# Performance work log

Measured on AMD Instinct MI355X. Metric: run time of the kernel, lower is better.

The kernel has to match this reference:

```python
import jax, jax.numpy as jnp
import numpy as np
from jax import lax

PRE_NMS_TOPN = 6000
POST_NMS_TOPN = 1500
NMS_IOU_THRESHOLD = 0.7
VARIANCES = (0.1, 0.1, 0.2, 0.2)
TOTAL_ANCHORS = 200000
BATCH = 8


def setup_inputs() -> dict:
    key = jax.random.key(0)
    k1, k2, k3, k4 = jax.random.split(key, 4)
    rpn_bbox_deltas = jax.random.normal(k1, (BATCH, TOTAL_ANCHORS, 4), dtype=jnp.float32)
    rpn_probs = jax.random.uniform(k2, (BATCH, TOTAL_ANCHORS), dtype=jnp.float32)
    # anchors: valid normalized [y1, x1, y2, x2] boxes
    ctr = jax.random.uniform(k3, (TOTAL_ANCHORS, 2), dtype=jnp.float32)          # (cy, cx)
    hw = jax.random.uniform(k4, (TOTAL_ANCHORS, 2), dtype=jnp.float32,
                            minval=0.02, maxval=0.3)                              # (h, w)
    anchors = jnp.concatenate([ctr - 0.5 * hw, ctr + 0.5 * hw], axis=-1)
    return {"rpn_bbox_deltas": rpn_bbox_deltas, "rpn_probs": rpn_probs, "anchors": anchors}


def _nms_single(boxes):
    # boxes: [P, 4] sorted by descending score; greedy NMS, return [POST, 4] zero-padded,
    # coordinates clipped to [0, 1] (tf combined_non_max_suppression clip_boxes=True default).
    P = boxes.shape[0]
    y1, x1, y2, x2 = boxes[:, 0], boxes[:, 1], boxes[:, 2], boxes[:, 3]
    area = (y2 - y1) * (x2 - x1)
    iy1 = jnp.maximum(y1[:, None], y1[None, :])
    ix1 = jnp.maximum(x1[:, None], x1[None, :])
    iy2 = jnp.minimum(y2[:, None], y2[None, :])
    ix2 = jnp.minimum(x2[:, None], x2[None, :])
    inter = jnp.maximum(iy2 - iy1, 0.0) * jnp.maximum(ix2 - ix1, 0.0)
    iou = inter / (area[:, None] + area[None, :] - inter)  # [P, P]
    idx = jnp.arange(P)

    def body(i, keep):
        suppressed = keep[i] & (iou[i] > NMS_IOU_THRESHOLD) & (idx > i)
        return keep & ~suppressed

    keep = lax.fori_loop(0, P, body, jnp.ones((P,), dtype=bool))

    rank = jnp.cumsum(keep) - 1                      # position among kept boxes
    valid = keep & (rank < POST_NMS_TOPN)
    tgt = jnp.where(valid, rank, POST_NMS_TOPN)      # overflow slot for dropped boxes
    clipped = jnp.clip(boxes, 0.0, 1.0)
    out = jnp.zeros((POST_NMS_TOPN + 1, 4), dtype=boxes.dtype)
    out = out.at[tgt].set(jnp.where(valid[:, None], clipped, 0.0))
    return out[:POST_NMS_TOPN]


def reference(rpn_bbox_deltas, rpn_probs, anchors):
    variances = jnp.asarray(VARIANCES, dtype=rpn_bbox_deltas.dtype)
    deltas = rpn_bbox_deltas * variances                       # [B, A, 4]

    anc_w = anchors[:, 3] - anchors[:, 1]
    anc_h = anchors[:, 2] - anchors[:, 0]
    anc_cx = anchors[:, 1] + 0.5 * anc_w
    anc_cy = anchors[:, 0] + 0.5 * anc_h

    bw = jnp.exp(deltas[..., 3]) * anc_w
    bh = jnp.exp(deltas[..., 2]) * anc_h
    bcx = deltas[..., 1] * anc_w + anc_cx
    bcy = deltas[..., 0] * anc_h + anc_cy

    y1 = bcy - 0.5 * bh
    x1 = bcx - 0.5 * bw
    y2 = bh + y1
    x2 = bw + x1
    rpn_bboxes = jnp.stack([y1, x1, y2, x2], axis=-1)          # [B, A, 4]

    _, pre_indices = lax.top_k(rpn_probs, PRE_NMS_TOPN)        # [B, P], sorted desc
    pre_boxes = jnp.take_along_axis(rpn_bboxes, pre_indices[..., None], axis=1)  # [B, P, 4]

    roi_bboxes = jax.vmap(_nms_single)(pre_boxes)              # [B, POST, 4]
    return roi_bboxes
```

## Files before the change

### kernel.cpp

```cpp
#include <hip/hip_runtime.h>
#include <hip/hip_bf16.h>


#define TOTAL   200000
#define NBATCH  8
#define PRE     6000
#define POST    1500
#define NW      94
#define CAP     8192
#define NQ      (TOTAL/4)
#define GR      256
#define NG      24
#define NGFAST  13
#define PLANES  960

__device__ __forceinline__ unsigned int prob_key(float p) {
    return __float_as_uint(__fadd_rn(p, 1.0f)) & 0x7FFFFFu;
}

__global__ __launch_bounds__(1024) void k_hist256(const float* __restrict__ probs,
                                                  unsigned int* __restrict__ hist) {
    const int b = blockIdx.y;
    const int tid = threadIdx.x;
    __shared__ unsigned int h[256];
    if (tid < 256) h[tid] = 0u;
    __syncthreads();
    const float4* p4 = (const float4*)(probs + (size_t)b * TOTAL);
    for (int i4 = blockIdx.x * 1024 + tid; i4 < NQ; i4 += 8 * 1024) {
        float4 v = p4[i4];
        atomicAdd(&h[prob_key(v.x) >> 15], 1u);
        atomicAdd(&h[prob_key(v.y) >> 15], 1u);
        atomicAdd(&h[prob_key(v.z) >> 15], 1u);
        atomicAdd(&h[prob_key(v.w) >> 15], 1u);
    }
    __syncthreads();
    if (tid < 256 && h[tid] > 0u) atomicAdd(&hist[b * 256 + tid], h[tid]);
}

__global__ __launch_bounds__(1024) void k_collect(const float* __restrict__ probs,
                                                  const unsigned int* __restrict__ hist,
                                                  unsigned long long* __restrict__ keys,
                                                  unsigned int* __restrict__ gcount) {
    const int b = blockIdx.y;
    const int tid = threadIdx.x;
    __shared__ unsigned int S[257];
    __shared__ unsigned int lcnt[256];
    __shared__ unsigned int gbase[256];
    __shared__ unsigned int s_B;
    if (tid == 0) { s_B = 0u; S[256] = 0u; }
    if (tid < 256) { S[tid] = hist[b * 256 + tid]; lcnt[tid] = 0u; }
    __syncthreads();
    for (int off = 1; off < 256; off <<= 1) {
        unsigned int v = 0u;
        if (tid < 256 && tid + off < 256) v = S[tid + off];
        __syncthreads();
        if (tid < 256) S[tid] += v;
        __syncthreads();
    }
    if (tid < 256 && S[tid] >= PRE) atomicMax(&s_B, (unsigned int)tid);
    __syncthreads();
    const unsigned int B = s_B;
    unsigned int kk[4], ii[4], tt[4], lp[4]; int n = 0;
    const int i4 = blockIdx.x * 1024 + tid;
    if (i4 < NQ) {
        float4 v = ((const float4*)(probs + (size_t)b * TOTAL))[i4];
        float pv[4] = {v.x, v.y, v.z, v.w};
#pragma unroll
        for (int j = 0; j < 4; ++j) {
            unsigned int key = prob_key(pv[j]);
            unsigned int t = key >> 15;
            if (t >= B) {
                kk[n] = key; ii[n] = (unsigned int)(i4 * 4 + j); tt[n] = t;
                lp[n] = atomicAdd(&lcnt[t], 1u);
                ++n;
            }
        }
    }
    __syncthreads();
    if (tid < 256 && lcnt[tid] > 0u)
        gbase[tid] = atomicAdd(&gcount[b * 256 + tid], lcnt[tid]);
    __syncthreads();
    for (int j = 0; j < n; ++j) {
        unsigned int t = tt[j];
        unsigned int pos = S[t + 1] + gbase[t] + lp[j];
        if (pos < CAP)
            keys[(size_t)b * CAP + pos] =
                ((unsigned long long)kk[j] << 32) | (unsigned long long)(~ii[j]);
    }
}

__global__ __launch_bounds__(256) void k_rank(const unsigned long long* __restrict__ keys,
                                              const unsigned int* __restrict__ hist,
                                              const float* __restrict__ deltas,
                                              const float* __restrict__ anchors,
                                              float4* __restrict__ boxes) {
    const int b   = blockIdx.y;
    const int rel = blockIdx.x;
    const int tid = threadIdx.x;
    __shared__ unsigned int S[257];
    __shared__ unsigned int s_B;
    __shared__ unsigned long long K2[CAP];
    __shared__ unsigned int CNT[512];
    __shared__ unsigned int W[512];
    __shared__ unsigned int P[256];
    if (tid == 0) { s_B = 0u; S[256] = 0u; }
    S[tid] = hist[b * 256 + tid];
    __syncthreads();
    for (int off = 1; off < 256; off <<= 1) {
        unsigned int v = (tid + off < 256) ? S[tid + off] : 0u;
        __syncthreads();
        S[tid] += v;
        __syncthreads();
    }
    if (S[tid] >= PRE) atomicMax(&s_B, (unsigned int)tid);
    __syncthreads();
    const int B = (int)s_B;
    const int t = B + rel;
    if (t > 255) return;
    const unsigned int lo = (rel == 15) ? 0u : S[t + 1];
    unsigned int hi = S[t]; if (hi > CAP) hi = CAP;
    if (hi <= lo) return;
    const unsigned int n = hi - lo;
    CNT[tid] = 0u; CNT[tid + 256] = 0u;
    __syncthreads();
    const unsigned long long* kb = keys + (size_t)b * CAP + lo;
    for (unsigned int i = tid; i < n; i += 256u) {
        const unsigned int key23 = (unsigned int)(kb[i] >> 32);
        const unsigned int bin = (rel == 15) ? (key23 >> 14) : ((key23 >> 6) & 511u);
        atomicAdd(&CNT[bin], 1u);
    }
    __syncthreads();
    {
        const unsigned int c0 = CNT[2 * tid], c1 = CNT[2 * tid + 1];
        P[tid] = c0 + c1;
        __syncthreads();
        for (int off = 1; off < 256; off <<= 1) {
            unsigned int v = (tid + off < 256) ? P[tid + off] : 0u;
            __syncthreads();
            P[tid] += v;
            __syncthreads();
        }
        const unsigned int above = P[tid] - (c0 + c1);
        W[2 * tid + 1] = above;
        W[2 * tid]     = above + c1;
    }
    __syncthreads();
    for (unsigned int i = tid; i < n; i += 256u) {
        const unsigned long long k = kb[i];
        const unsigned int key23 = (unsigned int)(k >> 32);
        const unsigned int bin = (rel == 15) ? (key23 >> 14) : ((key23 >> 6) & 511u);
        const unsigned int slot = atomicAdd(&W[bin], 1u);
        K2[slot] = k;
    }
    __syncthreads();
    for (int s = tid; s < 512; s += 256) {
        const unsigned int st = (s < 511) ? W[s + 1] : 0u;
        const unsigned int en = W[s];
        for (unsigned int x = st; x + 1 < en; ++x) {
            unsigned long long best = K2[x]; unsigned int bi = x;
            for (unsigned int y = x + 1; y < en; ++y) {
                unsigned long long v = K2[y];
                if (v > best) { best = v; bi = y; }
            }
            if (bi != x) { K2[bi] = K2[x]; K2[x] = best; }
        }
    }
    __syncthreads();
    for (unsigned int r = tid; r < n; r += 256u) {
        const unsigned int grank = lo + r;
        if (grank >= PRE) continue;
        const unsigned long long k = K2[r];
        const unsigned int idx = ~(unsigned int)(k & 0xFFFFFFFFull);
        const float* d = deltas + ((size_t)b * TOTAL + (size_t)idx) * 4;
        const float* a = anchors + (size_t)idx * 4;
        float d0 = __fmul_rn(d[0], 0.1f), d1 = __fmul_rn(d[1], 0.1f);
        float d2 = __fmul_rn(d[2], 0.2f), d3 = __fmul_rn(d[3], 0.2f);
        float a0 = a[0], a1 = a[1], a2 = a[2], a3 = a[3];
        float aw = __fsub_rn(a3, a1), ah = __fsub_rn(a2, a0);
        float acx = __fadd_rn(a1, __fmul_rn(0.5f, aw));
        float acy = __fadd_rn(a0, __fmul_rn(0.5f, ah));
        float bw = __fmul_rn(expf(d3), aw);
        float bh = __fmul_rn(expf(d2), ah);
        float bcx = __fadd_rn(__fmul_rn(d1, aw), acx);
        float bcy = __fadd_rn(__fmul_rn(d0, ah), acy);
        float y1 = __fsub_rn(bcy, __fmul_rn(0.5f, bh));
        float x1 = __fsub_rn(bcx, __fmul_rn(0.5f, bw));
        float y2 = __fadd_rn(bh, y1);
        float x2 = __fadd_rn(bw, x1);
        boxes[(size_t)b * PRE + grank] = make_float4(y1, x1, y2, x2);
    }
}

__global__ __launch_bounds__(256) void k_mask(const float4* __restrict__ boxes,
                                              unsigned long long* __restrict__ maskT) {
    const int b  = blockIdx.z;
    const int by = blockIdx.y;
    const int bx = blockIdx.x;
    if (bx < by) return;
    const int tid = threadIdx.x;
    __shared__ float4 cbox[256];
    __shared__ float  cth[256];
    __shared__ float  cca[256];
    {
        int col = bx * 256 + tid;
        float4 cb = (col < PRE) ? boxes[(size_t)b * PRE + col] : make_float4(0.f, 0.f, 0.f, 0.f);
        cbox[tid] = cb;
        float ca = __fmul_rn(__fsub_rn(cb.z, cb.x), __fsub_rn(cb.w, cb.y));
        cca[tid] = ca;
        cth[tid] = __fmul_rn(0.4115f, ca);
    }
    __syncthreads();
    const int il = tid & 63;
    const int ws = tid >> 6;
    const int w  = bx * 4 + ws;
    if (w >= NW) return;
    const int ibase = by * 256 + il;
    float4 rb0, rb1, rb2, rb3;
    {
        const float4 z = make_float4(0.f, 0.f, 0.f, 0.f);
        rb0 = boxes[(size_t)b * PRE + ibase];
        rb1 = (ibase +  64 < PRE) ? boxes[(size_t)b * PRE + ibase +  64] : z;
        rb2 = (ibase + 128 < PRE) ? boxes[(size_t)b * PRE + ibase + 128] : z;
        rb3 = (ibase + 192 < PRE) ? boxes[(size_t)b * PRE + ibase + 192] : z;
    }
    const float ra0 = __fmul_rn(__fsub_rn(rb0.z, rb0.x), __fsub_rn(rb0.w, rb0.y));
    const float ra1 = __fmul_rn(__fsub_rn(rb1.z, rb1.x), __fsub_rn(rb1.w, rb1.y));
    const float ra2 = __fmul_rn(__fsub_rn(rb2.z, rb2.x), __fsub_rn(rb2.w, rb2.y));
    const float ra3 = __fmul_rn(__fsub_rn(rb3.z, rb3.x), __fsub_rn(rb3.w, rb3.y));
    const float rc0 = __fmul_rn(0.4115f, ra0);
    const float rc1 = __fmul_rn(0.4115f, ra1);
    const float rc2 = __fmul_rn(0.4115f, ra2);
    const float rc3 = __fmul_rn(0.4115f, ra3);
    unsigned long long bits0 = 0ull, bits1 = 0ull, bits2 = 0ull, bits3 = 0ull;
    const double M = 0x1.666667p-1;
#pragma unroll 8
    for (int jj = 0; jj < 64; ++jj) {
        const float4 cb = cbox[ws * 64 + jj];
        const float  th = cth[ws * 64 + jj];
#define ROWTEST(rb, ra, rc, bits)                                              \
        {                                                                      \
            float dy = __fsub_rn(fminf(rb.z, cb.z), fmaxf(rb.x, cb.x));        \
            float dx = __fsub_rn(fminf(rb.w, cb.w), fmaxf(rb.y, cb.y));        \
            float hh = fmaxf(dy, 0.0f);                                        \
            float in = __fmul_rn(hh, dx);                                      \
            if (in > __fadd_rn(rc, th)) {                                      \
                float ww2 = fmaxf(dx, 0.0f);                                   \
                float ix  = __fmul_rn(hh, ww2);                                \
                float un  = __fsub_rn(__fadd_rn(ra, cca[ws * 64 + jj]), ix);   \
                if ((double)ix >= M * (double)un) bits |= (1ull << jj);        \
            }                                                                  \
        }
        ROWTEST(rb0, ra0, rc0, bits0)
        ROWTEST(rb1, ra1, rc1, bits1)
        ROWTEST(rb2, ra2, rc2, bits2)
        ROWTEST(rb3, ra3, rc3, bits3)
#undef ROWTEST
    }
    const int jbase = w * 64;
#define ROWSTORE(k, bits)                                                      \
    {                                                                          \
        const int i = ibase + 64 * (k);                                        \
        if (i < PRE && w >= (i >> 6)) {                                        \
            unsigned long long bb = bits;                                      \
            if (jbase <= i) {                                                  \
                int nclear = i - jbase + 1;                                    \
                bb = (nclear >= 64) ? 0ull : (bb & (~0ull << nclear));         \
            }                                                                  \
            maskT[((size_t)b * NW + w) * PRE + i] = bb;                        \
        }                                                                      \
    }
    ROWSTORE(0, bits0)
    ROWSTORE(1, bits1)
    ROWSTORE(2, bits2)
    ROWSTORE(3, bits3)
#undef ROWSTORE
}

__device__ __forceinline__ unsigned long long rfl64(unsigned long long v) {
    unsigned int lo = (unsigned int)__builtin_amdgcn_readfirstlane((unsigned int)v);
    unsigned int hi = (unsigned int)__builtin_amdgcn_readfirstlane((unsigned int)(v >> 32));
    return ((unsigned long long)hi << 32) | (unsigned long long)lo;
}

__device__ __forceinline__ unsigned long long shflxor64(unsigned long long v, int m) {
    unsigned int lo = (unsigned int)__shfl_xor((unsigned int)v, m, 64);
    unsigned int hi = (unsigned int)__shfl_xor((unsigned int)(v >> 32), m, 64);
    return ((unsigned long long)hi << 32) | (unsigned long long)lo;
}

__device__ __forceinline__ unsigned long long bfly_or64(unsigned long long v) {
    v |= shflxor64(v, 1);  v |= shflxor64(v, 2);  v |= shflxor64(v, 4);
    v |= shflxor64(v, 8);  v |= shflxor64(v, 16); v |= shflxor64(v, 32);
    return v;
}

#define DIDX(qr,qw) ((qr)*4 + (qw) - ((qr)*((qr)+1))/2)

__global__ __launch_bounds__(1024) void k_scan(const float4* __restrict__ boxes,
                                               const unsigned long long* __restrict__ maskT,
                                               float4* __restrict__ out) {
    const int b = blockIdx.x;
    const int tid = threadIdx.x;
    const int wv = tid >> 6;
    const int lane = tid & 63;
    __shared__ unsigned long long remw[2][4];
    __shared__ unsigned long long keptbm[96];
    __shared__ float4 boxbuf[2][GR];
    __shared__ float4 keptbox[POST];
    __shared__ unsigned int s_rank;
    __shared__ int s_done;
    __shared__ int s_sup;
    if (tid < 8) ((unsigned long long*)remw)[tid] = 0ull;
    if (tid < 96) keptbm[tid] = 0ull;
    if (tid == 0) { s_rank = 0u; s_done = 0; }
    const unsigned long long* mb = maskT + (size_t)b * NW * PRE;

    unsigned long long dCur[10];
    unsigned long long pend0 = 0ull, pend1 = 0ull;
    unsigned int rank = 0u;

    if (wv == 0) {
#pragma unroll
        for (int qr = 0; qr < 4; ++qr) {
            const int row = 64 * qr + lane;
#pragma unroll
            for (int qw = qr; qw < 4; ++qw)
                dCur[DIDX(qr, qw)] = mb[(size_t)qw * PRE + row];
        }
    } else if (wv == 1) {
#pragma unroll
        for (int q = 0; q < 4; ++q)
            boxbuf[0][64 * q + lane] = boxes[(size_t)b * PRE + 64 * q + lane];
    }
    __syncthreads();

    for (int g = 0; g < NGFAST; ++g) {
        const int r0 = g * GR;
        const int w0 = g * 4;
        if (wv > 0) {
            const int L = tid - 64;
            unsigned int* R = (unsigned int*)&remw[g & 1][0];
            if (pend0) {
                const int q = L >> 8;
                const int row = (g - 1) * GR + (L & 255);
                if ((keptbm[row >> 6] >> (row & 63)) & 1ull) {
                    atomicOr(&R[2 * q],     (unsigned int)pend0);
                    atomicOr(&R[2 * q + 1], (unsigned int)(pend0 >> 32));
                }
            }
            if (pend1) {
                const int row = (g - 1) * GR + 192 + L;
                if ((keptbm[row >> 6] >> (row & 63)) & 1ull) {
                    atomicOr(&R[6], (unsigned int)pend1);
                    atomicOr(&R[7], (unsigned int)(pend1 >> 32));
                }
            }
        }
        __syncthreads();

        if (wv == 0) {
            unsigned long long dNxt[10];
#pragma unroll
            for (int i = 0; i < 10; ++i) dNxt[i] = 0ull;
            if (g + 1 < NGFAST) {
                const int r0n = (g + 1) * GR, w0n = (g + 1) * 4;
#pragma unroll
                for (int qr = 0; qr < 4; ++qr) {
                    const int row = r0n + 64 * qr + lane;
                    const bool rok = row < PRE;
#pragma unroll
                    for (int qw = qr; qw < 4; ++qw) {
                        const int w = w0n + qw;
                        if (rok && w < NW)
                            dNxt[DIDX(qr, qw)] = mb[(size_t)w * PRE + row];
                    }
                }
            }
            unsigned long long av[4];
#pragma unroll
            for (int q = 0; q < 4; ++q) av[q] = remw[g & 1][q];
            if (lane < 4) remw[g & 1][lane] = 0ull;
#pragma unroll
            for (int q = 0; q < 4; ++q) {
                const int rq = r0 + 64 * q;
                const unsigned long long valid =
                    (rq >= PRE) ? 0ull
                    : ((rq + 64 <= PRE) ? ~0ull : ((~0ull) >> (64 - (PRE - rq))));
                av[q] = rfl64(~av[q]) & valid;
            }
            unsigned long long keptq[4];
            unsigned int base = rank;
#pragma unroll
            for (int q = 0; q < 4; ++q) {
                const unsigned long long avq = av[q];
                const unsigned long long W = dCur[DIDX(q, q)];
                unsigned long long kept = 0ull;
                if (avq != 0ull) {
                    unsigned long long m = ((avq >> lane) & 1ull) ? W : 0ull;
                    const unsigned long long U = rfl64(bfly_or64(m));
                    const unsigned long long C = avq & ~U;
                    kept = C;
                    unsigned long long rem = avq & U;
                    if (rem != 0ull) {
                        unsigned long long mc = ((C >> lane) & 1ull) ? W : 0ull;
                        const unsigned long long UC = rfl64(bfly_or64(mc));
                        unsigned long long av2 = rem & ~UC;
                        const unsigned int wlo = (unsigned int)W;
                        const unsigned int whi = (unsigned int)(W >> 32);
                        while (av2) {
                            const int i2 = __ffsll((long long)av2) - 1;
                            const unsigned long long bit = 1ull << i2;
                            kept |= bit;
                            const unsigned long long Wi =
                                ((unsigned long long)(unsigned int)__builtin_amdgcn_readlane(whi, i2) << 32)
                                | (unsigned long long)(unsigned int)__builtin_amdgcn_readlane(wlo, i2);
                            av2 &= ~(Wi | bit);
                        }
                    }
                }
                keptq[q] = kept;
                if (q < 3 && kept != 0ull) {
                    const bool on = ((kept >> lane) & 1ull) != 0ull;
                    unsigned long long c1 = 0ull, c2 = 0ull, c3 = 0ull;
                    if (q == 0 && on) { c1 = dCur[DIDX(0,1)]; c2 = dCur[DIDX(0,2)]; c3 = dCur[DIDX(0,3)]; }
                    if (q == 1 && on) { c2 = dCur[DIDX(1,2)]; c3 = dCur[DIDX(1,3)]; }
                    if (q == 2 && on) { c3 = dCur[DIDX(2,3)]; }
#pragma unroll
                    for (int ms = 1; ms < 64; ms <<= 1) {
                        if (q == 0) c1 |= shflxor64(c1, ms);
                        if (q <= 1) c2 |= shflxor64(c2, ms);
                        c3 |= shflxor64(c3, ms);
                    }
                    if (q == 0) av[1] &= ~rfl64(c1);
                    if (q <= 1) av[2] &= ~rfl64(c2);
                    av[3] &= ~rfl64(c3);
                }
                if ((kept >> lane) & 1ull) {
                    const unsigned int r =
                        base + (unsigned int)__popcll(kept & ((1ull << lane) - 1ull));
                    if (r < POST) {
                        const float4 v = boxbuf[g & 1][64 * q + lane];
                        keptbox[r] = v;
                        float4 cl;
                        cl.x = fminf(fmaxf(v.x, 0.f), 1.f);
                        cl.y = fminf(fmaxf(v.y, 0.f), 1.f);
                        cl.z = fminf(fmaxf(v.z, 0.f), 1.f);
                        cl.w = fminf(fmaxf(v.w, 0.f), 1.f);
                        out[(size_t)b * POST + r] = cl;
                    }
                }
                base += (unsigned int)__popcll(kept);
            }
            if (lane == 0) {
                keptbm[w0 + 0] = keptq[0];
                keptbm[w0 + 1] = keptq[1];
                keptbm[w0 + 2] = keptq[2];
                keptbm[w0 + 3] = keptq[3];
                s_rank = base;
                s_done = (base >= POST) ? 1 : 0;
            }
            rank = base;
#pragma unroll
            for (int i = 0; i < 10; ++i) dCur[i] = dNxt[i];
        } else {
            const int L = tid - 64;
            pend0 = 0ull; pend1 = 0ull;
            if (g + 1 < NGFAST) {
                const int w0n = (g + 1) * 4;
                if (wv == 1) {
#pragma unroll
                    for (int q = 0; q < 4; ++q) {
                        const int row = (g + 1) * GR + 64 * q + lane;
                        boxbuf[(g + 1) & 1][64 * q + lane] =
                            (row < PRE) ? boxes[(size_t)b * PRE + row]
                                        : make_float4(0.f, 0.f, 0.f, 0.f);
                    }
                }
                const bool ok1 = (w0n + 1 < NW), ok2 = (w0n + 2 < NW), ok3 = (w0n + 3 < NW);
                unsigned long long a0 = 0ull, a1 = 0ull, a2 = 0ull, a3 = 0ull;
                const int rlim = g * GR;
                for (int row = L; row < rlim; row += PLANES) {
                    const unsigned long long km =
                        ((keptbm[row >> 6] >> (row & 63)) & 1ull) ? ~0ull : 0ull;
                    const unsigned long long* cb = mb + row;
                    const unsigned long long v0 = cb[(size_t)(w0n + 0) * PRE];
                    const unsigned long long v1 = ok1 ? cb[(size_t)(w0n + 1) * PRE] : 0ull;
                    const unsigned long long v2 = ok2 ? cb[(size_t)(w0n + 2) * PRE] : 0ull;
                    const unsigned long long v3 = ok3 ? cb[(size_t)(w0n + 3) * PRE] : 0ull;
                    a0 |= v0 & km; a1 |= v1 & km; a2 |= v2 & km; a3 |= v3 & km;
                }
                {
                    unsigned int* R = (unsigned int*)&remw[(g + 1) & 1][0];
                    if (a0) { atomicOr(&R[0], (unsigned int)a0); atomicOr(&R[1], (unsigned int)(a0 >> 32)); }
                    if (a1) { atomicOr(&R[2], (unsigned int)a1); atomicOr(&R[3], (unsigned int)(a1 >> 32)); }
                    if (a2) { atomicOr(&R[4], (unsigned int)a2); atomicOr(&R[5], (unsigned int)(a2 >> 32)); }
                    if (a3) { atomicOr(&R[6], (unsigned int)a3); atomicOr(&R[7], (unsigned int)(a3 >> 32)); }
                }
                {
                    const int q = L >> 8;
                    const int w = w0n + q;
                    if (w < NW)
                        pend0 = mb[(size_t)w * PRE + (size_t)(g * GR + (L & 255))];
                }
                if (L < 64) {
                    const int w = w0n + 3;
                    if (w < NW)
                        pend1 = mb[(size_t)w * PRE + (size_t)(g * GR + 192 + L)];
                }
            }
        }
        __syncthreads();
        if (s_done) break;
    }

    if (!s_done) {
        unsigned int rk = s_rank;
        const double M = 0x1.666667p-1;
        for (int row = NGFAST * GR; row < PRE && rk < POST; ++row) {
            if (tid == 0) s_sup = 0;
            __syncthreads();
            const float4 rb = boxes[(size_t)b * PRE + row];
            const float ra = __fmul_rn(__fsub_rn(rb.z, rb.x), __fsub_rn(rb.w, rb.y));
            int sup = 0;
            for (unsigned int j = (unsigned int)tid; j < rk; j += 1024u) {
                const float4 kb = keptbox[j];
                float dy = __fsub_rn(fminf(rb.z, kb.z), fmaxf(rb.x, kb.x));
                float dx = __fsub_rn(fminf(rb.w, kb.w), fmaxf(rb.y, kb.y));
                float hh = fmaxf(dy, 0.f);
                float ww = fmaxf(dx, 0.f);
                float ix = __fmul_rn(hh, ww);
                float ka = __fmul_rn(__fsub_rn(kb.z, kb.x), __fsub_rn(kb.w, kb.y));
                float un = __fsub_rn(__fadd_rn(ka, ra), ix);
                if ((double)ix >= M * (double)un) { sup = 1; break; }
            }
            if (sup) atomicOr(&s_sup, 1);
            __syncthreads();
            if (!s_sup) {
                if (tid == 0) {
                    keptbox[rk] = rb;
                    float4 cl;
                    cl.x = fminf(fmaxf(rb.x, 0.f), 1.f);
                    cl.y = fminf(fmaxf(rb.y, 0.f), 1.f);
                    cl.z = fminf(fmaxf(rb.z, 0.f), 1.f);
                    cl.w = fminf(fmaxf(rb.w, 0.f), 1.f);
                    out[(size_t)b * POST + rk] = cl;
                }
                ++rk;
                __syncthreads();
            }
        }
        if (tid == 0) s_rank = rk;
        __syncthreads();
    }

    unsigned int filled = s_rank; if (filled > POST) filled = POST;
    for (unsigned int r = filled + (unsigned int)tid; r < POST; r += 1024u)
        out[(size_t)b * POST + r] = make_float4(0.f, 0.f, 0.f, 0.f);
}

extern "C" void kernel_launch(void* const* d_in, const int* in_sizes, int n_in,
                              void* d_out, int out_size, void* d_ws, size_t ws_size,
                              hipStream_t stream) {
    const float* deltas  = (const float*)d_in[0];
    const float* probs   = (const float*)d_in[1];
    const float* anchors = (const float*)d_in[2];
    char* ws = (char*)d_ws;
    unsigned int*       hist   = (unsigned int*)(ws);
    unsigned int*       gcount = (unsigned int*)(ws + 8192);
    unsigned long long* keys   = (unsigned long long*)(ws + 16384);
    float4*             boxes  = (float4*)(ws + 16384 + 524288);
    unsigned long long* maskT  = (unsigned long long*)(ws + 16384 + 524288 + 768000);
    float4* out = (float4*)d_out;

    hipMemsetAsync(ws, 0, 16384, stream);
    k_hist256<<<dim3(8, NBATCH), 1024, 0, stream>>>(probs, hist);
    k_collect<<<dim3((NQ + 1023) / 1024, NBATCH), 1024, 0, stream>>>(probs, hist, keys, gcount);
    k_rank<<<dim3(16, NBATCH), 256, 0, stream>>>(keys, hist, deltas, anchors, boxes);
    k_mask<<<dim3(NGFAST, NGFAST, NBATCH), 256, 0, stream>>>(boxes, maskT);
    k_scan<<<NBATCH, 1024, 0, stream>>>(boxes, maskT, out);
}
```

Before: 156.1 us.

## Drop memset via per-block histograms, swizzle-based wave OR, shrink mask grid

Each histogram block now writes its own partial histogram, and the consumers sum the 8 partials. This removes the hipMemsetAsync and the global atomics, and the gcount zeroing moves into the first kernel. The wave-wide 64-bit OR reduction in the NMS scan drops the shfl_xor butterfly for ds_swizzle steps within 32-lane halves plus two readlanes, which cuts per-step latency on the serial path. NGFAST shrinks from 13 to 9, which reduces the mask kernel grid and may mean fewer mask tiles are computed. That is a risk if the scan relies on the missing tiles.

```diff
diff --git a/kernel.cpp b/kernel.cpp
--- a/kernel.cpp
+++ b/kernel.cpp
@@ -10,8 +10,7 @@
 #define CAP     8192
 #define NQ      (TOTAL/4)
 #define GR      256
-#define NG      24
-#define NGFAST  13
+#define NGFAST  9
 #define PLANES  960
 
 __device__ __forceinline__ unsigned int prob_key(float p) {
@@ -19,14 +18,17 @@
 }
 
 __global__ __launch_bounds__(1024) void k_hist256(const float* __restrict__ probs,
-                                                  unsigned int* __restrict__ hist) {
+                                                  unsigned int* __restrict__ histS,
+                                                  unsigned int* __restrict__ gcount) {
     const int b = blockIdx.y;
+    const int bx = blockIdx.x;
     const int tid = threadIdx.x;
     __shared__ unsigned int h[256];
     if (tid < 256) h[tid] = 0u;
+    if (bx == 0 && tid < 256) gcount[b * 256 + tid] = 0u;
     __syncthreads();
     const float4* p4 = (const float4*)(probs + (size_t)b * TOTAL);
-    for (int i4 = blockIdx.x * 1024 + tid; i4 < NQ; i4 += 8 * 1024) {
+    for (int i4 = bx * 1024 + tid; i4 < NQ; i4 += 8 * 1024) {
         float4 v = p4[i4];
         atomicAdd(&h[prob_key(v.x) >> 15], 1u);
         atomicAdd(&h[prob_key(v.y) >> 15], 1u);
@@ -34,11 +36,11 @@
         atomicAdd(&h[prob_key(v.w) >> 15], 1u);
     }
     __syncthreads();
-    if (tid < 256 && h[tid] > 0u) atomicAdd(&hist[b * 256 + tid], h[tid]);
+    if (tid < 256) histS[((size_t)b * 8 + bx) * 256 + tid] = h[tid];
 }
 
 __global__ __launch_bounds__(1024) void k_collect(const float* __restrict__ probs,
-                                                  const unsigned int* __restrict__ hist,
+                                                  const unsigned int* __restrict__ histS,
                                                   unsigned long long* __restrict__ keys,
                                                   unsigned int* __restrict__ gcount) {
     const int b = blockIdx.y;
@@ -48,7 +50,13 @@
     __shared__ unsigned int gbase[256];
     __shared__ unsigned int s_B;
     if (tid == 0) { s_B = 0u; S[256] = 0u; }
-    if (tid < 256) { S[tid] = hist[b * 256 + tid]; lcnt[tid] = 0u; }
+    if (tid < 256) {
+        unsigned int s = 0u;
+        const unsigned int* hb = histS + (size_t)b * 8 * 256 + tid;
+#pragma unroll
+        for (int k = 0; k < 8; ++k) s += hb[k * 256];
+        S[tid] = s; lcnt[tid] = 0u;
+    }
     __syncthreads();
     for (int off = 1; off < 256; off <<= 1) {
         unsigned int v = 0u;
@@ -90,7 +98,7 @@
 }
 
 __global__ __launch_bounds__(256) void k_rank(const unsigned long long* __restrict__ keys,
-                                              const unsigned int* __restrict__ hist,
+                                              const unsigned int* __restrict__ histS,
                                               const float* __restrict__ deltas,
                                               const float* __restrict__ anchors,
                                               float4* __restrict__ boxes) {
@@ -104,7 +112,13 @@
     __shared__ unsigned int W[512];
     __shared__ unsigned int P[256];
     if (tid == 0) { s_B = 0u; S[256] = 0u; }
-    S[tid] = hist[b * 256 + tid];
+    {
+        unsigned int s = 0u;
+        const unsigned int* hb = histS + (size_t)b * 8 * 256 + tid;
+#pragma unroll
+        for (int k = 0; k < 8; ++k) s += hb[k * 256];
+        S[tid] = s;
+    }
     __syncthreads();
     for (int off = 1; off < 256; off <<= 1) {
         unsigned int v = (tid + off < 256) ? S[tid + off] : 0u;
@@ -282,16 +296,19 @@
     return ((unsigned long long)hi << 32) | (unsigned long long)lo;
 }
 
-__device__ __forceinline__ unsigned long long shflxor64(unsigned long long v, int m) {
-    unsigned int lo = (unsigned int)__shfl_xor((unsigned int)v, m, 64);
-    unsigned int hi = (unsigned int)__shfl_xor((unsigned int)(v >> 32), m, 64);
-    return ((unsigned long long)hi << 32) | (unsigned long long)lo;
-}
-
-__device__ __forceinline__ unsigned long long bfly_or64(unsigned long long v) {
-    v |= shflxor64(v, 1);  v |= shflxor64(v, 2);  v |= shflxor64(v, 4);
-    v |= shflxor64(v, 8);  v |= shflxor64(v, 16); v |= shflxor64(v, 32);
-    return v;
+__device__ __forceinline__ unsigned long long wor64(unsigned long long v) {
+    int lo = (int)(unsigned int)v;
+    int hi = (int)(unsigned int)(v >> 32);
+    lo |= __builtin_amdgcn_ds_swizzle(lo, 0x041F); hi |= __builtin_amdgcn_ds_swizzle(hi, 0x041F);
+    lo |= __builtin_amdgcn_ds_swizzle(lo, 0x081F); hi |= __builtin_amdgcn_ds_swizzle(hi, 0x081F);
+    lo |= __builtin_amdgcn_ds_swizzle(lo, 0x101F); hi |= __builtin_amdgcn_ds_swizzle(hi, 0x101F);
+    lo |= __builtin_amdgcn_ds_swizzle(lo, 0x201F); hi |= __builtin_amdgcn_ds_swizzle(hi, 0x201F);
+    lo |= __builtin_amdgcn_ds_swizzle(lo, 0x401F); hi |= __builtin_amdgcn_ds_swizzle(hi, 0x401F);
+    const unsigned int l = (unsigned int)__builtin_amdgcn_readlane(lo, 0)
+                         | (unsigned int)__builtin_amdgcn_readlane(lo, 32);
+    const unsigned int h = (unsigned int)__builtin_amdgcn_readlane(hi, 0)
+                         | (unsigned int)__builtin_amdgcn_readlane(hi, 32);
+    return ((unsigned long long)h << 32) | (unsigned long long)l;
 }
 
 #define DIDX(qr,qw) ((qr)*4 + (qw) - ((qr)*((qr)+1))/2)
@@ -397,13 +414,13 @@
                 unsigned long long kept = 0ull;
                 if (avq != 0ull) {
                     unsigned long long m = ((avq >> lane) & 1ull) ? W : 0ull;
-                    const unsigned long long U = rfl64(bfly_or64(m));
+                    const unsigned long long U = wor64(m);
                     const unsigned long long C = avq & ~U;
                     kept = C;
                     unsigned long long rem = avq & U;
                     if (rem != 0ull) {
                         unsigned long long mc = ((C >> lane) & 1ull) ? W : 0ull;
-                        const unsigned long long UC = rfl64(bfly_or64(mc));
+                        const unsigned long long UC = wor64(mc);
                         unsigned long long av2 = rem & ~UC;
                         const unsigned int wlo = (unsigned int)W;
                         const unsigned int whi = (unsigned int)(W >> 32);
@@ -425,15 +442,9 @@
                     if (q == 0 && on) { c1 = dCur[DIDX(0,1)]; c2 = dCur[DIDX(0,2)]; c3 = dCur[DIDX(0,3)]; }
                     if (q == 1 && on) { c2 = dCur[DIDX(1,2)]; c3 = dCur[DIDX(1,3)]; }
                     if (q == 2 && on) { c3 = dCur[DIDX(2,3)]; }
-#pragma unroll
-                    for (int ms = 1; ms < 64; ms <<= 1) {
-                        if (q == 0) c1 |= shflxor64(c1, ms);
-                        if (q <= 1) c2 |= shflxor64(c2, ms);
-                        c3 |= shflxor64(c3, ms);
-                    }
-                    if (q == 0) av[1] &= ~rfl64(c1);
-                    if (q <= 1) av[2] &= ~rfl64(c2);
-                    av[3] &= ~rfl64(c3);
+                    if (q == 0) av[1] &= ~wor64(c1);
+                    if (q <= 1) av[2] &= ~wor64(c2);
+                    av[3] &= ~wor64(c3);
                 }
                 if ((kept >> lane) & 1ull) {
                     const unsigned int r =
@@ -565,17 +576,16 @@
     const float* probs   = (const float*)d_in[1];
     const float* anchors = (const float*)d_in[2];
     char* ws = (char*)d_ws;
-    unsigned int*       hist   = (unsigned int*)(ws);
-    unsigned int*       gcount = (unsigned int*)(ws + 8192);
-    unsigned long long* keys   = (unsigned long long*)(ws + 16384);
-    float4*             boxes  = (float4*)(ws + 16384 + 524288);
-    unsigned long long* maskT  = (unsigned long long*)(ws + 16384 + 524288 + 768000);
+    unsigned int*       histS  = (unsigned int*)(ws);
+    unsigned int*       gcount = (unsigned int*)(ws + 65536);
+    unsigned long long* keys   = (unsigned long long*)(ws + 73728);
+    float4*             boxes  = (float4*)(ws + 73728 + 524288);
+    unsigned long long* maskT  = (unsigned long long*)(ws + 73728 + 524288 + 768000);
     float4* out = (float4*)d_out;
 
-    hipMemsetAsync(ws, 0, 16384, stream);
-    k_hist256<<<dim3(8, NBATCH), 1024, 0, stream>>>(probs, hist);
-    k_collect<<<dim3((NQ + 1023) / 1024, NBATCH), 1024, 0, stream>>>(probs, hist, keys, gcount);
-    k_rank<<<dim3(16, NBATCH), 256, 0, stream>>>(keys, hist, deltas, anchors, boxes);
+    k_hist256<<<dim3(8, NBATCH), 1024, 0, stream>>>(probs, histS, gcount);
+    k_collect<<<dim3((NQ + 1023) / 1024, NBATCH), 1024, 0, stream>>>(probs, histS, keys, gcount);
+    k_rank<<<dim3(16, NBATCH), 256, 0, stream>>>(keys, histS, deltas, anchors, boxes);
     k_mask<<<dim3(NGFAST, NGFAST, NBATCH), 256, 0, stream>>>(boxes, maskT);
     k_scan<<<NBATCH, 1024, 0, stream>>>(boxes, maskT, out);
 }
```

Measured after the change: 143.8 us. -7.9%, faster.
